# Optimization experiments

Measured on AMD Instinct MI355X. Metric: run time of the kernel, lower is better.

The kernel has to match this reference:

```python
import jax, jax.numpy as jnp
import numpy as np

LAN_DIM = 2048
FEA_DIM = 128
N = 65536
SHRINK_THRES = 0.0025
R = 1.0
EPS = 1e-12


def setup_inputs() -> dict:
    key = jax.random.key(0)
    k1, k2 = jax.random.split(key)
    x = jax.random.normal(k1, (N, FEA_DIM), dtype=jnp.float32)
    # reset_parameters: uniform(-stdv, stdv), stdv = 1/sqrt(fea_dim)
    stdv = 1.0 / np.sqrt(FEA_DIM)
    weight = jax.random.uniform(k2, (LAN_DIM, FEA_DIM), dtype=jnp.float32,
                                minval=-stdv, maxval=stdv)
    return {"input": x, "weight": weight}


def reference(input, weight):
    x = input                                    # [N, D]
    logits = jnp.einsum('nd,ld->nl', x, weight)  # [N, L]
    att = jax.nn.softmax(logits, axis=1)
    # hard_shrink_relu
    shifted = att - SHRINK_THRES
    att = jax.nn.relu(shifted) * att / (jnp.abs(shifted) + EPS)
    # F.normalize(p=1, dim=1): x / max(||x||_1, eps); att is nonneg
    att = att / jnp.maximum(jnp.sum(att, axis=1, keepdims=True), EPS)
    output = jnp.einsum('nl,ld->nd', att, weight)  # [N, D]

    # nearest landmark: argmax over att per sample
    ind = jnp.argmax(att, axis=1)                # [N]
    nl = weight[ind]                             # [N, D]
    # second-nearest: overwrite each row's argmax entry with the row min, re-argmax
    row_min = jnp.min(att, axis=1)               # [N]
    att2 = att.at[jnp.arange(N), ind].set(row_min)
    ind2 = jnp.argmax(att2, axis=1)
    nl2 = weight[ind2]                           # [N, D]

    # center of codebook, samples within radius R (boolean mask instead of
    # data-dependent-length index list, for jit compatibility)
    cen = jnp.mean(weight, axis=0)               # [D]
    dist = jnp.sqrt(jnp.sum((x - cen[None, :]) ** 2, axis=1))
    col = dist < R                               # [N] bool

    return output, att, nl, nl2, col
```

## Files before the change

### kernel.cpp

```cpp
#include <hip/hip_runtime.h>
#include <math.h>

#define NS 65536
#define LAN 2048
#define FEA 128

constexpr float THRES = 0.0025f;
constexpr float FEPS  = 1e-12f;
constexpr int BM   = 32;
constexpr int MAXS = 63;

typedef _Float16 half8 __attribute__((ext_vector_type(8)));
typedef float    f32x4 __attribute__((ext_vector_type(4)));

__global__ void k_prep(const float* __restrict__ W,
                       _Float16* __restrict__ Wh, _Float16* __restrict__ Wl,
                       float* __restrict__ censum) {
    if (blockIdx.x < 1024) {
        int i = blockIdx.x * 256 + threadIdx.x;
        float w = W[i];
        _Float16 h = (_Float16)w;
        Wh[i] = h;
        Wl[i] = (_Float16)(w - (float)h);
    } else {
        __shared__ f32x4 sred[8][32];
        const int b = blockIdx.x - 1024;
        const int tid = threadIdx.x;
        const int rg = tid >> 5, q = tid & 31;
        const f32x4* W4 = (const f32x4*)W;
        f32x4 p = (f32x4){0.f, 0.f, 0.f, 0.f};
        #pragma unroll
        for (int j = 0; j < 8; ++j) {
            int row = b * 64 + rg * 8 + j;
            p += W4[(size_t)row * 32 + q];
        }
        sred[rg][q] = p;
        __syncthreads();
        if (tid < 32) {
            f32x4 s = sred[0][tid];
            #pragma unroll
            for (int w = 1; w < 8; ++w) s += sred[w][tid];
            #pragma unroll
            for (int e = 0; e < 4; ++e)
                atomicAdd(&censum[tid * 4 + e], s[e]);
        }
    }
}

__device__ static inline void gload_lds16(const void* g, void* l) {
    __builtin_amdgcn_global_load_lds(
        (const __attribute__((address_space(1))) void*)g,
        (__attribute__((address_space(3))) void*)l, 16, 0, 0);
}

__global__ __launch_bounds__(512, 2) void k_main(
    const float* __restrict__ X,
    const _Float16* __restrict__ Wh, const _Float16* __restrict__ Wl,
    const float* __restrict__ censum,
    float* __restrict__ o_att, float* __restrict__ o_col)
{
    __shared__ __align__(16) char s_pool[147456];
    __shared__ float s_red[8][BM];
    __shared__ float s_rsinv[BM], s_Sinv[BM];
    __shared__ int   s_cnt[BM];

    const int tid  = threadIdx.x;
    const int wv   = tid >> 6;
    const int lane = tid & 63;
    const int g    = lane >> 4;
    const int m    = lane & 15;
    const int row0 = blockIdx.x * BM;
    constexpr int XOFF = 131072;

    #define ISSUE_BH(t_, buf_)                                                      \
        {                                                                           \
            const char* gh_ = (const char*)(Wh + (size_t)(wv * 256 + (t_) * 16) * FEA); \
            char* lb_ = s_pool + (buf_) * 65536 + wv * 8192;                        \
            _Pragma("unroll")                                                       \
            for (int i_ = 0; i_ < 4; ++i_) {                                        \
                int c_ = i_ * 64 + lane;                                            \
                int gc_ = c_ ^ ((c_ >> 4) & 7);                                     \
                gload_lds16(gh_ + gc_ * 16, lb_ + i_ * 1024);                       \
            }                                                                       \
        }
    #define ISSUE_BL(t_, buf_)                                                      \
        {                                                                           \
            const char* gl_ = (const char*)(Wl + (size_t)(wv * 256 + (t_) * 16) * FEA); \
            char* lb_ = s_pool + (buf_) * 65536 + wv * 8192 + 4096;                 \
            _Pragma("unroll")                                                       \
            for (int i_ = 0; i_ < 4; ++i_) {                                        \
                int c_ = i_ * 64 + lane;                                            \
                int gc_ = c_ ^ ((c_ >> 4) & 7);                                     \
                gload_lds16(gl_ + gc_ * 16, lb_ + i_ * 1024);                       \
            }                                                                       \
        }

    {
        const char* xg = (const char*)(X + (size_t)row0 * FEA);
        gload_lds16(xg + (wv * 2 + 0) * 1024 + lane * 16, s_pool + XOFF + (wv * 2 + 0) * 1024);
        gload_lds16(xg + (wv * 2 + 1) * 1024 + lane * 16, s_pool + XOFF + (wv * 2 + 1) * 1024);
    }
    ISSUE_BH(0, 0) ISSUE_BL(0, 0)
    ISSUE_BH(1, 1) ISSUE_BL(1, 1)
    asm volatile("s_waitcnt vmcnt(16)" ::: "memory");
    __builtin_amdgcn_s_barrier();
    __builtin_amdgcn_sched_barrier(0);

    half8 afh[2][4], afl[2][4];
    #pragma unroll
    for (int rt = 0; rt < 2; ++rt)
        #pragma unroll
        for (int kb = 0; kb < 4; ++kb) {
            const char* base = s_pool + XOFF + (rt * 16 + m) * 512 + (kb * 8 + g * 2) * 16;
            f32x4 xa = *(const f32x4*)(base);
            f32x4 xb = *(const f32x4*)(base + 16);
            half8 h, l;
            #pragma unroll
            for (int e = 0; e < 4; ++e) {
                _Float16 hh = (_Float16)xa[e];
                h[e] = hh; l[e] = (_Float16)(xa[e] - (float)hh);
            }
            #pragma unroll
            for (int e = 0; e < 4; ++e) {
                _Float16 hh = (_Float16)xb[e];
                h[4 + e] = hh; l[4 + e] = (_Float16)(xb[e] - (float)hh);
            }
            afh[rt][kb] = h; afl[rt][kb] = l;
        }

    const float inv2048 = 1.0f / 2048.0f;
    #pragma unroll
    for (int u = 0; u < 4; ++u) {
        const int lr = wv * 4 + u;
        float2 x2 = *(const float2*)(s_pool + XOFF + lr * 512 + lane * 8);
        float dx0 = x2.x - censum[lane * 2] * inv2048;
        float dx1 = x2.y - censum[lane * 2 + 1] * inv2048;
        float dd = dx0 * dx0 + dx1 * dx1;
        #pragma unroll
        for (int off = 32; off >= 1; off >>= 1) dd += __shfl_xor(dd, off);
        if (lane == 0) o_col[row0 + lr] = (sqrtf(dd) < 1.0f) ? 1.0f : 0.0f;
    }

    f32x4 acc[2][16];
    #pragma unroll
    for (int rt = 0; rt < 2; ++rt)
        #pragma unroll
        for (int t = 0; t < 16; ++t) acc[rt][t] = (f32x4){0.f, 0.f, 0.f, 0.f};
    float ssum[2][4];
    #pragma unroll
    for (int rt = 0; rt < 2; ++rt)
        #pragma unroll
        for (int r = 0; r < 4; ++r) ssum[rt][r] = 0.f;

    #pragma unroll 16
    for (int t = 0; t < 16; ++t) {
        const int buf = t & 1;
        const char* bb = s_pool + buf * 65536 + wv * 8192;
        if (t <= 14) { asm volatile("s_waitcnt vmcnt(12)" ::: "memory"); }
        else         { asm volatile("s_waitcnt vmcnt(4)"  ::: "memory"); }
        __builtin_amdgcn_sched_barrier(0);
        half8 bh[4];
        #pragma unroll
        for (int kb = 0; kb < 4; ++kb) {
            int off = (m * 256 + kb * 64 + g * 16) ^ ((m & 7) << 4);
            bh[kb] = *(const half8*)(bb + off);
        }
        asm volatile("s_waitcnt lgkmcnt(0)" ::: "memory");
        __builtin_amdgcn_sched_barrier(0);
        if (t < 14) ISSUE_BH(t + 2, buf)
        __builtin_amdgcn_s_setprio(1);
        #pragma unroll
        for (int kb = 0; kb < 4; ++kb)
            #pragma unroll
            for (int rt = 0; rt < 2; ++rt) {
                acc[rt][t] = __builtin_amdgcn_mfma_f32_16x16x32_f16(afh[rt][kb], bh[kb], acc[rt][t], 0, 0, 0);
                acc[rt][t] = __builtin_amdgcn_mfma_f32_16x16x32_f16(afl[rt][kb], bh[kb], acc[rt][t], 0, 0, 0);
            }
        __builtin_amdgcn_s_setprio(0);
        if (t <= 13)      { asm volatile("s_waitcnt vmcnt(12)" ::: "memory"); }
        else if (t == 14) { asm volatile("s_waitcnt vmcnt(8)"  ::: "memory"); }
        else              { asm volatile("s_waitcnt vmcnt(0)"  ::: "memory"); }
        __builtin_amdgcn_sched_barrier(0);
        half8 bl[4];
        #pragma unroll
        for (int kb = 0; kb < 4; ++kb) {
            int off = (m * 256 + kb * 64 + g * 16) ^ ((m & 7) << 4);
            bl[kb] = *(const half8*)(bb + 4096 + off);
        }
        asm volatile("s_waitcnt lgkmcnt(0)" ::: "memory");
        __builtin_amdgcn_sched_barrier(0);
        if (t < 14) ISSUE_BL(t + 2, buf)
        __builtin_amdgcn_s_setprio(1);
        #pragma unroll
        for (int kb = 0; kb < 4; ++kb)
            #pragma unroll
            for (int rt = 0; rt < 2; ++rt)
                acc[rt][t] = __builtin_amdgcn_mfma_f32_16x16x32_f16(afh[rt][kb], bl[kb], acc[rt][t], 0, 0, 0);
        __builtin_amdgcn_s_setprio(0);
        #pragma unroll
        for (int rt = 0; rt < 2; ++rt)
            #pragma unroll
            for (int r = 0; r < 4; ++r) {
                float e = __expf(acc[rt][t][r]);
                acc[rt][t][r] = e;
                ssum[rt][r] += e;
            }
    }
    #undef ISSUE_BH
    #undef ISSUE_BL


    #pragma unroll
    for (int rt = 0; rt < 2; ++rt)
        #pragma unroll
        for (int r = 0; r < 4; ++r) {
            float s = ssum[rt][r];
            #pragma unroll
            for (int off = 8; off >= 1; off >>= 1) s += __shfl_xor(s, off);
            if (m == 0) s_red[wv][rt*16 + g*4 + r] = s;
        }
    __syncthreads();
    if (tid < BM) {
        float s = s_red[0][tid];
        #pragma unroll
        for (int w = 1; w < 8; ++w) s += s_red[w][tid];
        s_rsinv[tid] = 1.0f / s;
        s_cnt[tid] = 0;
    }
    __syncthreads();

    int*   s_scol = (int*)s_pool;
    float* s_sval = (float*)(s_pool + 16384);
    #pragma unroll
    for (int rt = 0; rt < 2; ++rt)
        #pragma unroll
        for (int r = 0; r < 4; ++r) {
            const int lr = rt*16 + g*4 + r;
            const float ri = s_rsinv[lr];
            float S = 0.f;
            #pragma unroll
            for (int t = 0; t < 16; ++t) {
                float soft = acc[rt][t][r] * ri;
                float sh = soft - THRES;
                if (sh > 0.f) {
                    float v = sh * soft / (sh + FEPS);
                    S += v;
                    int p = atomicAdd(&s_cnt[lr], 1);
                    if (p < MAXS) { s_scol[lr*64 + p] = wv*256 + t*16 + m; s_sval[lr*64 + p] = v; }
                }
            }
            #pragma unroll
            for (int off = 8; off >= 1; off >>= 1) S += __shfl_xor(S, off);
            if (m == 0) s_red[wv][lr] = S;
        }
    __syncthreads();
    if (tid < BM) {
        float S = s_red[0][tid];
        #pragma unroll
        for (int w = 1; w < 8; ++w) S += s_red[w][tid];
        s_Sinv[tid] = 1.0f / fmaxf(S, FEPS);
    }
    __syncthreads();

    {
        const int lrp = tid >> 4, j = tid & 15;
        const int cn = min(s_cnt[lrp], MAXS);
        const float si = s_Sinv[lrp];
        f32x4 vq, cq;
        #pragma unroll
        for (int e = 0; e < 4; ++e) {
            int p = j * 4 + e;
            if (p == 63) {
                vq[e] = 0.f;
                cq[e] = __int_as_float(cn);
            } else {
                bool live = p < cn;
                vq[e] = live ? s_sval[lrp*64 + p] * si : 0.f;
                cq[e] = __int_as_float(live ? s_scol[lrp*64 + p] : 0);
            }
        }
        float* base = o_att + (size_t)(row0 + lrp) * LAN;
        *(f32x4*)(base + j * 4)      = vq;
        *(f32x4*)(base + 64 + j * 4) = cq;
    }
}

__global__ __launch_bounds__(256) void k_att(
    const float* __restrict__ W,
    float* __restrict__ o_att, float* __restrict__ o_out,
    float* __restrict__ o_nl, float* __restrict__ o_nl2)
{
    __shared__ float s_att[8 * 2048];
    __shared__ float s_pack[8][128];
    __shared__ int   s_i1[8], s_i2[8];

    const int tid = threadIdx.x;
    const size_t rows0 = (size_t)blockIdx.x * 8;
    const int row = tid >> 5, q = tid & 31;

    *(f32x4*)&s_pack[row][q * 4] = *(const f32x4*)(o_att + (rows0 + row) * LAN + q * 4);
    __syncthreads();

    if (tid < 8) {
        const float* pk = s_pack[tid];
        const int cnt = __float_as_int(pk[64 + 63]);
        float t1v = -1.f, t2v = -1.f; int t1c = 0x7fffffff, t2c = 0x7fffffff;
        for (int p = 0; p < cnt; ++p) {
            float v = pk[p]; int c = __float_as_int(pk[64 + p]);
            if (v > t1v || (v == t1v && c < t1c)) {
                t2v = t1v; t2c = t1c; t1v = v; t1c = c;
            } else if (v > t2v || (v == t2v && c < t2c)) {
                t2v = v; t2c = c;
            }
        }
        s_i1[tid] = (cnt >= 1) ? t1c : 0;
        s_i2[tid] = (cnt >= 2) ? t2c : 0;
    }
    f32x4* sa4 = (f32x4*)s_att;
    #pragma unroll
    for (int e = 0; e < 16; ++e) sa4[e * 256 + tid] = (f32x4){0.f, 0.f, 0.f, 0.f};
    __syncthreads();

    {
        const int cnt = __float_as_int(s_pack[row][64 + 63]);
        #pragma unroll
        for (int h = 0; h < 2; ++h) {
            int p = q + h * 32;
            if (p < cnt) {
                float v = s_pack[row][p];
                int c = __float_as_int(s_pack[row][64 + p]);
                s_att[row * 2048 + c] = v;
            }
        }
        f32x4 o = (f32x4){0.f, 0.f, 0.f, 0.f};
        for (int p = 0; p < cnt; ++p) {
            float v = s_pack[row][p];
            int c = __float_as_int(s_pack[row][64 + p]);
            const f32x4 w4 = *(const f32x4*)(W + (size_t)c * FEA + q * 4);
            o += v * w4;
        }
        __builtin_nontemporal_store(o, (f32x4*)(o_out + (rows0 + row) * FEA + q * 4));
        const int i1 = s_i1[row], i2 = s_i2[row];
        __builtin_nontemporal_store(*(const f32x4*)(W + (size_t)i1 * FEA + q * 4),
                                    (f32x4*)(o_nl  + (rows0 + row) * FEA + q * 4));
        __builtin_nontemporal_store(*(const f32x4*)(W + (size_t)i2 * FEA + q * 4),
                                    (f32x4*)(o_nl2 + (rows0 + row) * FEA + q * 4));
    }
    __syncthreads();

    float* gdst = o_att + rows0 * LAN;
    #pragma unroll
    for (int e = 0; e < 16; ++e) {
        int fi = e * 256 + tid;
        __builtin_nontemporal_store(sa4[fi], (f32x4*)(gdst + (size_t)fi * 4));
    }
}

extern "C" void kernel_launch(void* const* d_in, const int* in_sizes, int n_in,
                              void* d_out, int out_size, void* d_ws, size_t ws_size,
                              hipStream_t stream) {
    const float* X = (const float*)d_in[0];
    const float* W = (const float*)d_in[1];

    _Float16* Wh = (_Float16*)d_ws;
    _Float16* Wl = Wh + (size_t)LAN * FEA;
    float*    censum = (float*)(Wl + (size_t)LAN * FEA);

    float* out      = (float*)d_out;
    float* o_output = out;
    float* o_att    = o_output + (size_t)NS * FEA;
    float* o_nl     = o_att    + (size_t)NS * LAN;
    float* o_nl2    = o_nl     + (size_t)NS * FEA;
    float* o_col    = o_nl2    + (size_t)NS * FEA;

    hipMemsetAsync(censum, 0, FEA * sizeof(float), stream);
    k_prep<<<1056, 256, 0, stream>>>(W, Wh, Wl, censum);
    k_main<<<NS / BM, 512, 0, stream>>>(X, Wh, Wl, censum, o_att, o_col);
    k_att<<<NS / 8, 256, 0, stream>>>(W, o_att, o_output, o_nl, o_nl2);
}
```

Before: 311.8 us.

## Share weight tiles across wave pairs with a 4-slot ring buffer

Waves are grouped in pairs. Each pair covers 512 landmark columns and each wave in the pair handles one 16-row tile. One wave loads the high-half fp16 weights and the other loads the low half into a shared slot, so the two waves split the global-to-LDS traffic. The double buffer becomes a 4-slot ring with three tiles in flight, and a block-wide barrier is added every iteration so that slots are safely reused. The aim is to cut per-wave load issue and A-fragment registers and to deepen prefetch. In exchange, every wave now reads both weight halves from LDS and the eight waves synchronize 32 times.

```diff
diff --git a/kernel.cpp b/kernel.cpp
--- a/kernel.cpp
+++ b/kernel.cpp
@@ -69,30 +69,22 @@
     const int lane = tid & 63;
     const int g    = lane >> 4;
     const int m    = lane & 15;
+    const int pair = wv >> 1;
+    const int rt   = wv & 1;
     const int row0 = blockIdx.x * BM;
     constexpr int XOFF = 131072;
 
-    #define ISSUE_BH(t_, buf_)                                                      \
-        {                                                                           \
-            const char* gh_ = (const char*)(Wh + (size_t)(wv * 256 + (t_) * 16) * FEA); \
-            char* lb_ = s_pool + (buf_) * 65536 + wv * 8192;                        \
-            _Pragma("unroll")                                                       \
-            for (int i_ = 0; i_ < 4; ++i_) {                                        \
-                int c_ = i_ * 64 + lane;                                            \
-                int gc_ = c_ ^ ((c_ >> 4) & 7);                                     \
-                gload_lds16(gh_ + gc_ * 16, lb_ + i_ * 1024);                       \
-            }                                                                       \
-        }
-    #define ISSUE_BL(t_, buf_)                                                      \
-        {                                                                           \
-            const char* gl_ = (const char*)(Wl + (size_t)(wv * 256 + (t_) * 16) * FEA); \
-            char* lb_ = s_pool + (buf_) * 65536 + wv * 8192 + 4096;                 \
-            _Pragma("unroll")                                                       \
-            for (int i_ = 0; i_ < 4; ++i_) {                                        \
-                int c_ = i_ * 64 + lane;                                            \
-                int gc_ = c_ ^ ((c_ >> 4) & 7);                                     \
-                gload_lds16(gl_ + gc_ * 16, lb_ + i_ * 1024);                       \
-            }                                                                       \
+    #define ISSUE_T(t_, slot_)                                                     \
+        {                                                                          \
+            const char* gsrc_ = (const char*)((rt ? Wl : Wh) +                     \
+                                 (size_t)(pair * 512 + (t_) * 16) * FEA);          \
+            char* lb_ = s_pool + (slot_) * 32768 + pair * 8192 + rt * 4096;        \
+            _Pragma("unroll")                                                      \
+            for (int i_ = 0; i_ < 4; ++i_) {                                       \
+                int c_ = i_ * 64 + lane;                                           \
+                int gc_ = c_ ^ ((c_ >> 4) & 7);                                    \
+                gload_lds16(gsrc_ + gc_ * 16, lb_ + i_ * 1024);                    \
+            }                                                                      \
         }
 
     {
@@ -100,33 +92,30 @@
         gload_lds16(xg + (wv * 2 + 0) * 1024 + lane * 16, s_pool + XOFF + (wv * 2 + 0) * 1024);
         gload_lds16(xg + (wv * 2 + 1) * 1024 + lane * 16, s_pool + XOFF + (wv * 2 + 1) * 1024);
     }
-    ISSUE_BH(0, 0) ISSUE_BL(0, 0)
-    ISSUE_BH(1, 1) ISSUE_BL(1, 1)
-    asm volatile("s_waitcnt vmcnt(16)" ::: "memory");
+    ISSUE_T(0, 0) ISSUE_T(1, 1) ISSUE_T(2, 2)
+    asm volatile("s_waitcnt vmcnt(12)" ::: "memory");
     __builtin_amdgcn_s_barrier();
     __builtin_amdgcn_sched_barrier(0);
 
-    half8 afh[2][4], afl[2][4];
-    #pragma unroll
-    for (int rt = 0; rt < 2; ++rt)
-        #pragma unroll
-        for (int kb = 0; kb < 4; ++kb) {
-            const char* base = s_pool + XOFF + (rt * 16 + m) * 512 + (kb * 8 + g * 2) * 16;
-            f32x4 xa = *(const f32x4*)(base);
-            f32x4 xb = *(const f32x4*)(base + 16);
-            half8 h, l;
-            #pragma unroll
-            for (int e = 0; e < 4; ++e) {
-                _Float16 hh = (_Float16)xa[e];
-                h[e] = hh; l[e] = (_Float16)(xa[e] - (float)hh);
-            }
-            #pragma unroll
-            for (int e = 0; e < 4; ++e) {
-                _Float16 hh = (_Float16)xb[e];
-                h[4 + e] = hh; l[4 + e] = (_Float16)(xb[e] - (float)hh);
-            }
-            afh[rt][kb] = h; afl[rt][kb] = l;
-        }
+    half8 afh[4], afl[4];
+    #pragma unroll
+    for (int kb = 0; kb < 4; ++kb) {
+        const char* base = s_pool + XOFF + (rt * 16 + m) * 512 + (kb * 8 + g * 2) * 16;
+        f32x4 xa = *(const f32x4*)(base);
+        f32x4 xb = *(const f32x4*)(base + 16);
+        half8 h, l;
+        #pragma unroll
+        for (int e = 0; e < 4; ++e) {
+            _Float16 hh = (_Float16)xa[e];
+            h[e] = hh; l[e] = (_Float16)(xa[e] - (float)hh);
+        }
+        #pragma unroll
+        for (int e = 0; e < 4; ++e) {
+            _Float16 hh = (_Float16)xb[e];
+            h[4 + e] = hh; l[4 + e] = (_Float16)(xb[e] - (float)hh);
+        }
+        afh[kb] = h; afl[kb] = l;
+    }
 
     const float inv2048 = 1.0f / 2048.0f;
     #pragma unroll
@@ -141,89 +130,59 @@
         if (lane == 0) o_col[row0 + lr] = (sqrtf(dd) < 1.0f) ? 1.0f : 0.0f;
     }
 
-    f32x4 acc[2][16];
-    #pragma unroll
-    for (int rt = 0; rt < 2; ++rt)
-        #pragma unroll
-        for (int t = 0; t < 16; ++t) acc[rt][t] = (f32x4){0.f, 0.f, 0.f, 0.f};
-    float ssum[2][4];
-    #pragma unroll
-    for (int rt = 0; rt < 2; ++rt)
-        #pragma unroll
-        for (int r = 0; r < 4; ++r) ssum[rt][r] = 0.f;
-
-    #pragma unroll 16
-    for (int t = 0; t < 16; ++t) {
-        const int buf = t & 1;
-        const char* bb = s_pool + buf * 65536 + wv * 8192;
-        if (t <= 14) { asm volatile("s_waitcnt vmcnt(12)" ::: "memory"); }
-        else         { asm volatile("s_waitcnt vmcnt(4)"  ::: "memory"); }
+    f32x4 acc[32];
+    #pragma unroll
+    for (int t = 0; t < 32; ++t) acc[t] = (f32x4){0.f, 0.f, 0.f, 0.f};
+    float ssum[4] = {0.f, 0.f, 0.f, 0.f};
+
+    #pragma unroll 32
+    for (int t = 0; t < 32; ++t) {
+        if (t <= 29)      { asm volatile("s_waitcnt vmcnt(8)" ::: "memory"); }
+        else if (t == 30) { asm volatile("s_waitcnt vmcnt(4)" ::: "memory"); }
+        else              { asm volatile("s_waitcnt vmcnt(0)" ::: "memory"); }
         __builtin_amdgcn_sched_barrier(0);
-        half8 bh[4];
+        __builtin_amdgcn_s_barrier();
+        __builtin_amdgcn_sched_barrier(0);
+        if (t < 29) ISSUE_T(t + 3, (t + 3) & 3)
+        const char* bb = s_pool + (t & 3) * 32768 + pair * 8192;
+        half8 bh[4], bl[4];
         #pragma unroll
         for (int kb = 0; kb < 4; ++kb) {
             int off = (m * 256 + kb * 64 + g * 16) ^ ((m & 7) << 4);
             bh[kb] = *(const half8*)(bb + off);
+            bl[kb] = *(const half8*)(bb + 4096 + off);
         }
         asm volatile("s_waitcnt lgkmcnt(0)" ::: "memory");
         __builtin_amdgcn_sched_barrier(0);
-        if (t < 14) ISSUE_BH(t + 2, buf)
         __builtin_amdgcn_s_setprio(1);
         #pragma unroll
-        for (int kb = 0; kb < 4; ++kb)
-            #pragma unroll
-            for (int rt = 0; rt < 2; ++rt) {
-                acc[rt][t] = __builtin_amdgcn_mfma_f32_16x16x32_f16(afh[rt][kb], bh[kb], acc[rt][t], 0, 0, 0);
-                acc[rt][t] = __builtin_amdgcn_mfma_f32_16x16x32_f16(afl[rt][kb], bh[kb], acc[rt][t], 0, 0, 0);
-            }
+        for (int kb = 0; kb < 4; ++kb) {
+            acc[t] = __builtin_amdgcn_mfma_f32_16x16x32_f16(afh[kb], bh[kb], acc[t], 0, 0, 0);
+            acc[t] = __builtin_amdgcn_mfma_f32_16x16x32_f16(afl[kb], bh[kb], acc[t], 0, 0, 0);
+            acc[t] = __builtin_amdgcn_mfma_f32_16x16x32_f16(afh[kb], bl[kb], acc[t], 0, 0, 0);
+        }
         __builtin_amdgcn_s_setprio(0);
-        if (t <= 13)      { asm volatile("s_waitcnt vmcnt(12)" ::: "memory"); }
-        else if (t == 14) { asm volatile("s_waitcnt vmcnt(8)"  ::: "memory"); }
-        else              { asm volatile("s_waitcnt vmcnt(0)"  ::: "memory"); }
-        __builtin_amdgcn_sched_barrier(0);
-        half8 bl[4];
-        #pragma unroll
-        for (int kb = 0; kb < 4; ++kb) {
-            int off = (m * 256 + kb * 64 + g * 16) ^ ((m & 7) << 4);
-            bl[kb] = *(const half8*)(bb + 4096 + off);
-        }
-        asm volatile("s_waitcnt lgkmcnt(0)" ::: "memory");
-        __builtin_amdgcn_sched_barrier(0);
-        if (t < 14) ISSUE_BL(t + 2, buf)
-        __builtin_amdgcn_s_setprio(1);
-        #pragma unroll
-        for (int kb = 0; kb < 4; ++kb)
-            #pragma unroll
-            for (int rt = 0; rt < 2; ++rt)
-                acc[rt][t] = __builtin_amdgcn_mfma_f32_16x16x32_f16(afh[rt][kb], bl[kb], acc[rt][t], 0, 0, 0);
-        __builtin_amdgcn_s_setprio(0);
-        #pragma unroll
-        for (int rt = 0; rt < 2; ++rt)
-            #pragma unroll
-            for (int r = 0; r < 4; ++r) {
-                float e = __expf(acc[rt][t][r]);
-                acc[rt][t][r] = e;
-                ssum[rt][r] += e;
-            }
-    }
-    #undef ISSUE_BH
-    #undef ISSUE_BL
-
-
-    #pragma unroll
-    for (int rt = 0; rt < 2; ++rt)
         #pragma unroll
         for (int r = 0; r < 4; ++r) {
-            float s = ssum[rt][r];
-            #pragma unroll
-            for (int off = 8; off >= 1; off >>= 1) s += __shfl_xor(s, off);
-            if (m == 0) s_red[wv][rt*16 + g*4 + r] = s;
-        }
+            float e = __expf(acc[t][r]);
+            acc[t][r] = e;
+            ssum[r] += e;
+        }
+    }
+    #undef ISSUE_T
+
+
+    #pragma unroll
+    for (int r = 0; r < 4; ++r) {
+        float s = ssum[r];
+        #pragma unroll
+        for (int off = 8; off >= 1; off >>= 1) s += __shfl_xor(s, off);
+        if (m == 0) s_red[wv][rt * 16 + g * 4 + r] = s;
+    }
     __syncthreads();
     if (tid < BM) {
-        float s = s_red[0][tid];
-        #pragma unroll
-        for (int w = 1; w < 8; ++w) s += s_red[w][tid];
+        const int b = tid >> 4;
+        float s = s_red[b][tid] + s_red[b + 2][tid] + s_red[b + 4][tid] + s_red[b + 6][tid];
         s_rsinv[tid] = 1.0f / s;
         s_cnt[tid] = 0;
     }
@@ -232,32 +191,29 @@
     int*   s_scol = (int*)s_pool;
     float* s_sval = (float*)(s_pool + 16384);
     #pragma unroll
-    for (int rt = 0; rt < 2; ++rt)
-        #pragma unroll
-        for (int r = 0; r < 4; ++r) {
-            const int lr = rt*16 + g*4 + r;
-            const float ri = s_rsinv[lr];
-            float S = 0.f;
-            #pragma unroll
-            for (int t = 0; t < 16; ++t) {
-                float soft = acc[rt][t][r] * ri;
-                float sh = soft - THRES;
-                if (sh > 0.f) {
-                    float v = sh * soft / (sh + FEPS);
-                    S += v;
-                    int p = atomicAdd(&s_cnt[lr], 1);
-                    if (p < MAXS) { s_scol[lr*64 + p] = wv*256 + t*16 + m; s_sval[lr*64 + p] = v; }
-                }
+    for (int r = 0; r < 4; ++r) {
+        const int lr = rt * 16 + g * 4 + r;
+        const float ri = s_rsinv[lr];
+        float S = 0.f;
+        #pragma unroll
+        for (int t = 0; t < 32; ++t) {
+            float soft = acc[t][r] * ri;
+            float sh = soft - THRES;
+            if (sh > 0.f) {
+                float v = sh * soft / (sh + FEPS);
+                S += v;
+                int p = atomicAdd(&s_cnt[lr], 1);
+                if (p < MAXS) { s_scol[lr * 64 + p] = pair * 512 + t * 16 + m; s_sval[lr * 64 + p] = v; }
             }
-            #pragma unroll
-            for (int off = 8; off >= 1; off >>= 1) S += __shfl_xor(S, off);
-            if (m == 0) s_red[wv][lr] = S;
-        }
+        }
+        #pragma unroll
+        for (int off = 8; off >= 1; off >>= 1) S += __shfl_xor(S, off);
+        if (m == 0) s_red[wv][lr] = S;
+    }
     __syncthreads();
     if (tid < BM) {
-        float S = s_red[0][tid];
-        #pragma unroll
-        for (int w = 1; w < 8; ++w) S += s_red[w][tid];
+        const int b = tid >> 4;
+        float S = s_red[b][tid] + s_red[b + 2][tid] + s_red[b + 4][tid] + s_red[b + 6][tid];
         s_Sinv[tid] = 1.0f / fmaxf(S, FEPS);
     }
     __syncthreads();
@@ -275,8 +231,8 @@
                 cq[e] = __int_as_float(cn);
             } else {
                 bool live = p < cn;
-                vq[e] = live ? s_sval[lrp*64 + p] * si : 0.f;
-                cq[e] = __int_as_float(live ? s_scol[lrp*64 + p] : 0);
+                vq[e] = live ? s_sval[lrp * 64 + p] * si : 0.f;
+                cq[e] = __int_as_float(live ? s_scol[lrp * 64 + p] : 0);
             }
         }
         float* base = o_att + (size_t)(row0 + lrp) * LAN;
```

After: 336.5 us. 1.08x slower.

## Split MFMA accumulator chains and defer exp to overlap with next tile

Applied to the files above, without the earlier changes.

The single serial MFMA accumulation chain per tile is split into three independent chains (hi*hi, lo*hi, hi*lo), summed afterwards. This shortens the dependency chain through the MFMA pipeline. The exp/softmax-sum for tile t is also moved into the next iteration, behind the LDS loads, so the transcendental work can overlap with memory waits and the MFMA stream. In exchange it needs extra accumulator registers and a slightly different summation order.

```diff
diff --git a/kernel.cpp b/kernel.cpp
--- a/kernel.cpp
+++ b/kernel.cpp
@@ -146,11 +146,13 @@
     for (int rt = 0; rt < 2; ++rt)
         #pragma unroll
         for (int t = 0; t < 16; ++t) acc[rt][t] = (f32x4){0.f, 0.f, 0.f, 0.f};
+    f32x4 tmpA[2], tmpB[2];
     float ssum[2][4];
     #pragma unroll
     for (int rt = 0; rt < 2; ++rt)
         #pragma unroll
         for (int r = 0; r < 4; ++r) ssum[rt][r] = 0.f;
+    const f32x4 fz = (f32x4){0.f, 0.f, 0.f, 0.f};
 
     #pragma unroll 16
     for (int t = 0; t < 16; ++t) {
@@ -165,17 +167,33 @@
             int off = (m * 256 + kb * 64 + g * 16) ^ ((m & 7) << 4);
             bh[kb] = *(const half8*)(bb + off);
         }
+        if (t > 0) {
+            #pragma unroll
+            for (int rt = 0; rt < 2; ++rt) {
+                f32x4 v = acc[rt][t - 1] + tmpA[rt] + tmpB[rt];
+                #pragma unroll
+                for (int r = 0; r < 4; ++r) {
+                    float e = __expf(v[r]);
+                    acc[rt][t - 1][r] = e;
+                    ssum[rt][r] += e;
+                }
+            }
+        }
         asm volatile("s_waitcnt lgkmcnt(0)" ::: "memory");
         __builtin_amdgcn_sched_barrier(0);
         if (t < 14) ISSUE_BH(t + 2, buf)
         __builtin_amdgcn_s_setprio(1);
-        #pragma unroll
-        for (int kb = 0; kb < 4; ++kb)
-            #pragma unroll
-            for (int rt = 0; rt < 2; ++rt) {
-                acc[rt][t] = __builtin_amdgcn_mfma_f32_16x16x32_f16(afh[rt][kb], bh[kb], acc[rt][t], 0, 0, 0);
-                acc[rt][t] = __builtin_amdgcn_mfma_f32_16x16x32_f16(afl[rt][kb], bh[kb], acc[rt][t], 0, 0, 0);
-            }
+        acc[0][t] = __builtin_amdgcn_mfma_f32_16x16x32_f16(afh[0][0], bh[0], acc[0][t], 0, 0, 0);
+        acc[1][t] = __builtin_amdgcn_mfma_f32_16x16x32_f16(afh[1][0], bh[0], acc[1][t], 0, 0, 0);
+        tmpA[0]   = __builtin_amdgcn_mfma_f32_16x16x32_f16(afl[0][0], bh[0], fz, 0, 0, 0);
+        tmpA[1]   = __builtin_amdgcn_mfma_f32_16x16x32_f16(afl[1][0], bh[0], fz, 0, 0, 0);
+        #pragma unroll
+        for (int kb = 1; kb < 4; ++kb) {
+            acc[0][t] = __builtin_amdgcn_mfma_f32_16x16x32_f16(afh[0][kb], bh[kb], acc[0][t], 0, 0, 0);
+            acc[1][t] = __builtin_amdgcn_mfma_f32_16x16x32_f16(afh[1][kb], bh[kb], acc[1][t], 0, 0, 0);
+            tmpA[0]   = __builtin_amdgcn_mfma_f32_16x16x32_f16(afl[0][kb], bh[kb], tmpA[0], 0, 0, 0);
+            tmpA[1]   = __builtin_amdgcn_mfma_f32_16x16x32_f16(afl[1][kb], bh[kb], tmpA[1], 0, 0, 0);
+        }
         __builtin_amdgcn_s_setprio(0);
         if (t <= 13)      { asm volatile("s_waitcnt vmcnt(12)" ::: "memory"); }
         else if (t == 14) { asm volatile("s_waitcnt vmcnt(8)"  ::: "memory"); }
@@ -191,20 +209,24 @@
         __builtin_amdgcn_sched_barrier(0);
         if (t < 14) ISSUE_BL(t + 2, buf)
         __builtin_amdgcn_s_setprio(1);
-        #pragma unroll
-        for (int kb = 0; kb < 4; ++kb)
-            #pragma unroll
-            for (int rt = 0; rt < 2; ++rt)
-                acc[rt][t] = __builtin_amdgcn_mfma_f32_16x16x32_f16(afh[rt][kb], bl[kb], acc[rt][t], 0, 0, 0);
+        tmpB[0] = __builtin_amdgcn_mfma_f32_16x16x32_f16(afh[0][0], bl[0], fz, 0, 0, 0);
+        tmpB[1] = __builtin_amdgcn_mfma_f32_16x16x32_f16(afh[1][0], bl[0], fz, 0, 0, 0);
+        #pragma unroll
+        for (int kb = 1; kb < 4; ++kb) {
+            tmpB[0] = __builtin_amdgcn_mfma_f32_16x16x32_f16(afh[0][kb], bl[kb], tmpB[0], 0, 0, 0);
+            tmpB[1] = __builtin_amdgcn_mfma_f32_16x16x32_f16(afh[1][kb], bl[kb], tmpB[1], 0, 0, 0);
+        }
         __builtin_amdgcn_s_setprio(0);
-        #pragma unroll
-        for (int rt = 0; rt < 2; ++rt)
-            #pragma unroll
-            for (int r = 0; r < 4; ++r) {
-                float e = __expf(acc[rt][t][r]);
-                acc[rt][t][r] = e;
-                ssum[rt][r] += e;
-            }
+    }
+    #pragma unroll
+    for (int rt = 0; rt < 2; ++rt) {
+        f32x4 v = acc[rt][15] + tmpA[rt] + tmpB[rt];
+        #pragma unroll
+        for (int r = 0; r < 4; ++r) {
+            float e = __expf(v[r]);
+            acc[rt][15][r] = e;
+            ssum[rt][r] += e;
+        }
     }
     #undef ISSUE_BH
     #undef ISSUE_BL
```

Result: slower. 664.7 us (+113.2%).

## Fuse sparse attention expansion, output gather and top-2 into main kernel

Applied to the files above, without the earlier changes.

Drops the separate k_att kernel. k_main now finds the top-2 indices from the sparse survivor lists already in LDS, computes the sparse att·W output and the nl/nl2 gathers directly, and expands the dense att rows through an LDS staging buffer in four phases. This avoids writing the packed sparse list to global memory and reading it back, and saves one kernel launch. In exchange k_main does more serial epilogue work per block with extra barriers, which could lower overlap, and the top-2 scan runs on only 32 threads.

```diff
diff --git a/kernel.cpp b/kernel.cpp
--- a/kernel.cpp
+++ b/kernel.cpp
@@ -53,16 +53,22 @@
         (__attribute__((address_space(3))) void*)l, 16, 0, 0);
 }
 
+#define RAWBAR() { asm volatile("s_waitcnt lgkmcnt(0)" ::: "memory"); \
+                   __builtin_amdgcn_s_barrier(); \
+                   __builtin_amdgcn_sched_barrier(0); }
+
 __global__ __launch_bounds__(512, 2) void k_main(
-    const float* __restrict__ X,
+    const float* __restrict__ X, const float* __restrict__ W,
     const _Float16* __restrict__ Wh, const _Float16* __restrict__ Wl,
     const float* __restrict__ censum,
-    float* __restrict__ o_att, float* __restrict__ o_col)
+    float* __restrict__ o_out, float* __restrict__ o_att,
+    float* __restrict__ o_nl, float* __restrict__ o_nl2,
+    float* __restrict__ o_col)
 {
     __shared__ __align__(16) char s_pool[147456];
     __shared__ float s_red[8][BM];
     __shared__ float s_rsinv[BM], s_Sinv[BM];
-    __shared__ int   s_cnt[BM];
+    __shared__ int   s_ind[BM], s_ind2[BM], s_cnt[BM];
 
     const int tid  = threadIdx.x;
     const int wv   = tid >> 6;
@@ -259,100 +265,64 @@
         #pragma unroll
         for (int w = 1; w < 8; ++w) S += s_red[w][tid];
         s_Sinv[tid] = 1.0f / fmaxf(S, FEPS);
-    }
-    __syncthreads();
-
-    {
-        const int lrp = tid >> 4, j = tid & 15;
-        const int cn = min(s_cnt[lrp], MAXS);
-        const float si = s_Sinv[lrp];
-        f32x4 vq, cq;
-        #pragma unroll
-        for (int e = 0; e < 4; ++e) {
-            int p = j * 4 + e;
-            if (p == 63) {
-                vq[e] = 0.f;
-                cq[e] = __int_as_float(cn);
-            } else {
-                bool live = p < cn;
-                vq[e] = live ? s_sval[lrp*64 + p] * si : 0.f;
-                cq[e] = __int_as_float(live ? s_scol[lrp*64 + p] : 0);
-            }
-        }
-        float* base = o_att + (size_t)(row0 + lrp) * LAN;
-        *(f32x4*)(base + j * 4)      = vq;
-        *(f32x4*)(base + 64 + j * 4) = cq;
-    }
-}
-
-__global__ __launch_bounds__(256) void k_att(
-    const float* __restrict__ W,
-    float* __restrict__ o_att, float* __restrict__ o_out,
-    float* __restrict__ o_nl, float* __restrict__ o_nl2)
-{
-    __shared__ float s_att[8 * 2048];
-    __shared__ float s_pack[8][128];
-    __shared__ int   s_i1[8], s_i2[8];
-
-    const int tid = threadIdx.x;
-    const size_t rows0 = (size_t)blockIdx.x * 8;
-    const int row = tid >> 5, q = tid & 31;
-
-    *(f32x4*)&s_pack[row][q * 4] = *(const f32x4*)(o_att + (rows0 + row) * LAN + q * 4);
-    __syncthreads();
-
-    if (tid < 8) {
-        const float* pk = s_pack[tid];
-        const int cnt = __float_as_int(pk[64 + 63]);
+        const int cn = min(s_cnt[tid], MAXS);
         float t1v = -1.f, t2v = -1.f; int t1c = 0x7fffffff, t2c = 0x7fffffff;
-        for (int p = 0; p < cnt; ++p) {
-            float v = pk[p]; int c = __float_as_int(pk[64 + p]);
+        for (int p = 0; p < cn; ++p) {
+            float v = s_sval[tid*64 + p]; int c = s_scol[tid*64 + p];
             if (v > t1v || (v == t1v && c < t1c)) {
                 t2v = t1v; t2c = t1c; t1v = v; t1c = c;
             } else if (v > t2v || (v == t2v && c < t2c)) {
                 t2v = v; t2c = c;
             }
         }
-        s_i1[tid] = (cnt >= 1) ? t1c : 0;
-        s_i2[tid] = (cnt >= 2) ? t2c : 0;
-    }
-    f32x4* sa4 = (f32x4*)s_att;
-    #pragma unroll
-    for (int e = 0; e < 16; ++e) sa4[e * 256 + tid] = (f32x4){0.f, 0.f, 0.f, 0.f};
+        s_ind[tid]  = (cn >= 1) ? t1c : 0;
+        s_ind2[tid] = (cn >= 2) ? t2c : 0;
+    }
     __syncthreads();
 
-    {
-        const int cnt = __float_as_int(s_pack[row][64 + 63]);
-        #pragma unroll
-        for (int h = 0; h < 2; ++h) {
-            int p = q + h * 32;
-            if (p < cnt) {
-                float v = s_pack[row][p];
-                int c = __float_as_int(s_pack[row][64 + p]);
-                s_att[row * 2048 + c] = v;
-            }
-        }
-        f32x4 o = (f32x4){0.f, 0.f, 0.f, 0.f};
-        for (int p = 0; p < cnt; ++p) {
-            float v = s_pack[row][p];
-            int c = __float_as_int(s_pack[row][64 + p]);
-            const f32x4 w4 = *(const f32x4*)(W + (size_t)c * FEA + q * 4);
-            o += v * w4;
-        }
-        __builtin_nontemporal_store(o, (f32x4*)(o_out + (rows0 + row) * FEA + q * 4));
-        const int i1 = s_i1[row], i2 = s_i2[row];
-        __builtin_nontemporal_store(*(const f32x4*)(W + (size_t)i1 * FEA + q * 4),
-                                    (f32x4*)(o_nl  + (rows0 + row) * FEA + q * 4));
-        __builtin_nontemporal_store(*(const f32x4*)(W + (size_t)i2 * FEA + q * 4),
-                                    (f32x4*)(o_nl2 + (rows0 + row) * FEA + q * 4));
-    }
-    __syncthreads();
-
-    float* gdst = o_att + rows0 * LAN;
-    #pragma unroll
-    for (int e = 0; e < 16; ++e) {
-        int fi = e * 256 + tid;
-        __builtin_nontemporal_store(sa4[fi], (f32x4*)(gdst + (size_t)fi * 4));
+    #pragma unroll
+    for (int u = 0; u < 4; ++u) {
+        const int lr = wv*4 + u;
+        const int grow = row0 + lr;
+        const int d0 = lane * 2;
+        const int cnt = min(s_cnt[lr], MAXS);
+        const float si = s_Sinv[lr];
+        float o0 = 0.f, o1 = 0.f;
+        for (int s2 = 0; s2 < cnt; ++s2) {
+            const int c = s_scol[lr*64 + s2];
+            const float v = s_sval[lr*64 + s2];
+            const float2 w2 = *(const float2*)(W + (size_t)c * FEA + d0);
+            o0 += v * w2.x; o1 += v * w2.y;
+        }
+        *(float2*)(o_out + (size_t)grow * FEA + d0) = make_float2(o0 * si, o1 * si);
+        const int i1 = s_ind[lr], i2 = s_ind2[lr];
+        *(float2*)(o_nl  + (size_t)grow * FEA + d0) = *(const float2*)(W + (size_t)i1 * FEA + d0);
+        *(float2*)(o_nl2 + (size_t)grow * FEA + d0) = *(const float2*)(W + (size_t)i2 * FEA + d0);
+    }
+
+    float* comp  = (float*)(s_pool + 32768);
+    f32x4* comp4 = (f32x4*)comp;
+    const f32x4 fz4 = (f32x4){0.f, 0.f, 0.f, 0.f};
+    #pragma unroll
+    for (int ph = 0; ph < 4; ++ph) {
+        #pragma unroll
+        for (int e = 0; e < 8; ++e) comp4[e * 512 + tid] = fz4;
+        RAWBAR();
+        {
+            const int lr = ph * 8 + wv;
+            const int cn = min(s_cnt[lr], MAXS);
+            const float si = s_Sinv[lr];
+            for (int p = lane; p < cn; p += 64)
+                comp[(wv << 11) + s_scol[lr*64 + p]] = s_sval[lr*64 + p] * si;
+        }
+        RAWBAR();
+        float* gdst = o_att + (size_t)(row0 + ph * 8) * LAN;
+        #pragma unroll
+        for (int e = 0; e < 8; ++e) {
+            int fi = e * 512 + tid;
+            __builtin_nontemporal_store(comp4[fi], (f32x4*)gdst + fi);
+        }
+        RAWBAR();
     }
 }
 
@@ -375,6 +345,6 @@
 
     hipMemsetAsync(censum, 0, FEA * sizeof(float), stream);
     k_prep<<<1056, 256, 0, stream>>>(W, Wh, Wl, censum);
-    k_main<<<NS / BM, 512, 0, stream>>>(X, Wh, Wl, censum, o_att, o_col);
-    k_att<<<NS / 8, 256, 0, stream>>>(W, o_att, o_output, o_nl, o_nl2);
+    k_main<<<NS / BM, 512, 0, stream>>>(X, W, Wh, Wl, censum,
+                                        o_output, o_att, o_nl, o_nl2, o_col);
 }
```

Result: faster. 296.0 us (-5.1%).
